# Performance work log

Hardware: AMD Instinct MI355X
Metric: run time of the kernel (lower is better)

The kernel has to match this reference:

```python
import jax, jax.numpy as jnp
import numpy as np

N = 50000      # num_nodes
R = 8          # num_relations
FIN = 128      # in_channels
H = 128        # hidden_channels
E = 800000     # num_edges (avg degree 16)


def _xavier(key, shape):
    fan_in, fan_out = shape[-2], shape[-1]
    lim = np.sqrt(6.0 / (fan_in + fan_out)).astype(np.float32)
    return jax.random.uniform(key, shape, jnp.float32, -lim, lim)


def setup_inputs() -> dict:
    key = jax.random.key(0)
    ks = jax.random.split(key, 10)
    return {
        "x": jax.random.normal(ks[0], (N, FIN), jnp.float32),
        "edge_index": jax.random.randint(ks[1], (2, E), 0, N, jnp.int32),
        "edge_type": jax.random.randint(ks[2], (E,), 0, R, jnp.int32),
        "rel_w0": _xavier(ks[3], (R, FIN, H)),
        "root_w0": _xavier(ks[4], (FIN, H)),
        "bias0": jnp.zeros((H,), jnp.float32),
        "rel_w1": _xavier(ks[5], (R, H, H)),
        "root_w1": _xavier(ks[6], (H, H)),
        "bias1": jnp.zeros((H,), jnp.float32),
        "rel_emb": _xavier(ks[7], (R, H)),
    }


def _rgcn_conv(x, src, dst, etype, rel_w, root_w, bias):
    # RGCNConv (PyG, aggr='mean'): out_i = root(x_i) + sum_r W_r * mean_{j in N_r(i)} x_j
    n = x.shape[0]
    seg = dst * R + etype                                   # fused (node, relation) segment id
    msgs = x[src]                                           # [E, F] gather
    sums = jax.ops.segment_sum(msgs, seg, num_segments=n * R)
    cnt = jax.ops.segment_sum(jnp.ones((src.shape[0], 1), x.dtype), seg, num_segments=n * R)
    mean = (sums / jnp.maximum(cnt, 1.0)).reshape(n, R, -1)  # [N, R, F]
    return jnp.einsum('nrf,rfh->nh', mean, rel_w) + x @ root_w + bias


def reference(x, edge_index, edge_type, rel_w0, root_w0, bias0,
              rel_w1, root_w1, bias1, rel_emb):
    src, dst = edge_index[0], edge_index[1]
    h = _rgcn_conv(x, src, dst, edge_type, rel_w0, root_w0, bias0)
    h = jax.nn.relu(h)  # dropout in eval mode (identity)
    h = _rgcn_conv(h, src, dst, edge_type, rel_w1, root_w1, bias1)
    return (h, rel_emb)
```

## Files before the change

kernel.cpp:

```cpp
#include <hip/hip_runtime.h>

typedef unsigned short ushort_t;
typedef __attribute__((ext_vector_type(8))) short short8;
typedef __attribute__((ext_vector_type(4))) float f32x4;
typedef __attribute__((ext_vector_type(4))) int int4v;

#define RNUM 8
#define FDIM 128
#define KDIM 1152

__device__ __forceinline__ float bf2f(ushort_t u) {
    union { unsigned int i; float f; } x;
    x.i = ((unsigned int)u) << 16;
    return x.f;
}
__device__ __forceinline__ ushort_t f2bf(float f) {
    union { float f; unsigned int i; } x;
    x.f = f;
    unsigned int u = x.i;
    u += 0x7fffu + ((u >> 16) & 1u);
    return (ushort_t)(u >> 16);
}

__device__ __forceinline__ void gl_lds16(const void* g, void* s) {
    __builtin_amdgcn_global_load_lds(
        (const __attribute__((address_space(1))) unsigned int*)g,
        (__attribute__((address_space(3))) unsigned int*)s, 16, 0, 0);
}


__global__ void init_head(int* __restrict__ head, int n) {
    int i = blockIdx.x * 256 + threadIdx.x;
    if (i < n) head[i] = -1;
}

__global__ void link_kernel(const int* __restrict__ src, const int* __restrict__ dst,
                            const int* __restrict__ et,
                            int* head, int2* __restrict__ meta, int E) {
    int i = blockIdx.x * 256 + threadIdx.x;
    if (i < E) {
        int seg = dst[i] * RNUM + et[i];
        int prev = atomicExch(&head[seg * 4 + (i & 3)], i);
        meta[i] = make_int2(src[i], prev);
    }
}


__global__ __launch_bounds__(256) void transpose_w(const float* __restrict__ rel_w,
                                                   const float* __restrict__ root_w,
                                                   ushort_t* __restrict__ Wt) {
    int r = blockIdx.x;
    const float* src = (r < 8) ? (rel_w + r * 16384) : root_w;
    __shared__ ushort_t t[128 * 130];
    for (int idx = threadIdx.x; idx < 16384; idx += 256)
        t[(idx >> 7) * 130 + (idx & 127)] = f2bf(src[idx]);
    __syncthreads();
    ushort_t* d = Wt + r * 16384;
    for (int idx = threadIdx.x; idx < 16384; idx += 256)
        d[idx] = t[(idx & 127) * 130 + (idx >> 7)];
}


__global__ void cast_x(const float* __restrict__ x, ushort_t* __restrict__ Mx, int total) {
    int i = (blockIdx.x * 256 + threadIdx.x) * 8;
    if (i >= total) return;
    float4 v0 = *(const float4*)(x + i);
    float4 v1 = *(const float4*)(x + i + 4);
    ushort_t o[8] = {f2bf(v0.x), f2bf(v0.y), f2bf(v0.z), f2bf(v0.w),
                     f2bf(v1.x), f2bf(v1.y), f2bf(v1.z), f2bf(v1.w)};
    int row = i >> 7, col = i & 127;
    *(int4v*)(Mx + (size_t)row * KDIM + 1024 + col) = *(int4v*)o;
}


__global__ __launch_bounds__(256) void seg_mean(const int4v* __restrict__ head4,
                                                const int2* __restrict__ meta,
                                                ushort_t* Mx, int NSEG) {
    int t = blockIdx.x * 256 + threadIdx.x;
    int seg = t >> 4;
    int l16 = t & 15;
    if (seg >= NSEG) return;
    const ushort_t* gbase = Mx + 1024 + (size_t)l16 * 8;

    float acc[8];
#pragma unroll
    for (int k = 0; k < 8; ++k) acc[k] = 0.f;

    int4v h4 = head4[seg];
    int j[4], s[4], n[4];
#pragma unroll
    for (int c = 0; c < 4; ++c) j[c] = h4[c];
#pragma unroll
    for (int c = 0; c < 4; ++c)
        if (j[c] >= 0) { int2 m = meta[j[c]]; s[c] = m.x; n[c] = m.y; }

    int cnt = 0;
    while ((j[0] & j[1] & j[2] & j[3]) >= 0) {
        int4v v[4];
#pragma unroll
        for (int c = 0; c < 4; ++c)
            if (j[c] >= 0) v[c] = *(const int4v*)(gbase + (size_t)s[c] * KDIM);
        int2 m2[4];
#pragma unroll
        for (int c = 0; c < 4; ++c)
            if (j[c] >= 0 && n[c] >= 0) m2[c] = meta[n[c]];
#pragma unroll
        for (int c = 0; c < 4; ++c) {
            if (j[c] >= 0) {
                const ushort_t* p = (const ushort_t*)&v[c];
#pragma unroll
                for (int k = 0; k < 8; ++k) acc[k] += bf2f(p[k]);
                ++cnt;
                j[c] = n[c];
                s[c] = m2[c].x;
                n[c] = m2[c].y;
            }
        }
    }

    float sc = (cnt > 0) ? 1.0f / (float)cnt : 0.f;
    ushort_t ov[8];
#pragma unroll
    for (int k = 0; k < 8; ++k) ov[k] = f2bf(acc[k] * sc);
    *(int4v*)(Mx + (size_t)(seg >> 3) * KDIM + (seg & 7) * 128 + l16 * 8) = *(int4v*)ov;
}


template <bool FINAL>
__global__ __launch_bounds__(256) void rgcn_gemm(
    const ushort_t* Mx, const ushort_t* __restrict__ Wt,
    const float* __restrict__ bias, float* __restrict__ outF,
    ushort_t* MxOut, int N) {
    __shared__ ushort_t As[128 * 128];
    __shared__ ushort_t Bs[128 * 128];
    int tid = threadIdx.x;
    int wid = tid >> 6, lane = tid & 63;
    int l16 = lane & 15, q = lane >> 4;
    int nodeBase = blockIdx.x * 128;

    f32x4 acc[2][8];
#pragma unroll
    for (int rt = 0; rt < 2; ++rt)
#pragma unroll
        for (int ct = 0; ct < 8; ++ct) acc[rt][ct] = (f32x4){0.f, 0.f, 0.f, 0.f};

    for (int r = 0; r < 9; ++r) {
        __syncthreads();
#pragma unroll
        for (int i = 0; i < 8; ++i) {
            int L = i * 256 + tid;
            int row = L >> 4;
            int c = (L & 15) ^ (row & 15);
            gl_lds16(Mx + (size_t)(nodeBase + row) * KDIM + r * 128 + c * 8,
                     (char*)As + (size_t)L * 16);
            gl_lds16(Wt + r * 16384 + row * 128 + c * 8,
                     (char*)Bs + (size_t)L * 16);
        }
        __syncthreads();
#pragma unroll
        for (int s = 0; s < 4; ++s) {
            int pos = ((s * 4 + q) ^ l16) * 16;
            short8 a0 = *(const short8*)((const char*)As + ((2 * wid + 0) * 16 + l16) * 256 + pos);
            short8 a1 = *(const short8*)((const char*)As + ((2 * wid + 1) * 16 + l16) * 256 + pos);
#pragma unroll
            for (int ct = 0; ct < 8; ++ct) {
                short8 b = *(const short8*)((const char*)Bs + (ct * 16 + l16) * 256 + pos);
                acc[0][ct] = __builtin_amdgcn_mfma_f32_16x16x32_bf16(a0, b, acc[0][ct], 0, 0, 0);
                acc[1][ct] = __builtin_amdgcn_mfma_f32_16x16x32_bf16(a1, b, acc[1][ct], 0, 0, 0);
            }
        }
    }
#pragma unroll
    for (int rt = 0; rt < 2; ++rt) {
#pragma unroll
        for (int ct = 0; ct < 8; ++ct) {
            int h = ct * 16 + l16;
            float bv = bias[h];
#pragma unroll
            for (int reg = 0; reg < 4; ++reg) {
                int node = nodeBase + (2 * wid + rt) * 16 + q * 4 + reg;
                if (node < N) {
                    float v = acc[rt][ct][reg] + bv;
                    if (FINAL) {
                        outF[(size_t)node * FDIM + h] = v;
                    } else {
                        v = fmaxf(v, 0.f);
                        MxOut[(size_t)node * KDIM + 1024 + h] = f2bf(v);
                    }
                }
            }
        }
    }
}

__global__ void copy_emb(const float* __restrict__ e, float* __restrict__ out, int n) {
    int i = blockIdx.x * 256 + threadIdx.x;
    if (i < n) out[i] = e[i];
}


extern "C" void kernel_launch(void* const* d_in, const int* in_sizes, int n_in,
                              void* d_out, int out_size, void* d_ws, size_t ws_size,
                              hipStream_t stream) {
    const float* x        = (const float*)d_in[0];
    const int* edge_index = (const int*)d_in[1];
    const int* edge_type  = (const int*)d_in[2];
    const float* rel_w0   = (const float*)d_in[3];
    const float* root_w0  = (const float*)d_in[4];
    const float* bias0    = (const float*)d_in[5];
    const float* rel_w1   = (const float*)d_in[6];
    const float* root_w1  = (const float*)d_in[7];
    const float* bias1    = (const float*)d_in[8];
    const float* rel_emb  = (const float*)d_in[9];

    int N = in_sizes[0] / FDIM;
    int E = in_sizes[1] / 2;
    int NSEG = N * RNUM;
    const int* src = edge_index;
    const int* dst = edge_index + E;

    int nb_gemm = (N + 127) / 128;
    int NPAD = nb_gemm * 128;

    char* w = (char*)d_ws;
    auto alloc = [&](size_t bytes) -> char* {
        char* p = w;
        w += (bytes + 255) & ~(size_t)255;
        return p;
    };
    int* head    = (int*)alloc((size_t)NSEG * 4 * 4);
    int2* meta   = (int2*)alloc((size_t)E * 8);
    ushort_t* Wt = (ushort_t*)alloc((size_t)2 * 9 * 16384 * 2);
    ushort_t* Mx = (ushort_t*)alloc((size_t)NPAD * KDIM * 2);
    (void)ws_size; (void)n_in; (void)out_size;

    int nb_head = (NSEG * 4 + 255) / 256;
    int nb_E    = (E + 255) / 256;
    int nb_mean = (NSEG * 16) / 256;
    int nb_cast = (N * FDIM) / (256 * 8);

    init_head<<<nb_head, 256, 0, stream>>>(head, NSEG * 4);
    link_kernel<<<nb_E, 256, 0, stream>>>(src, dst, edge_type, head, meta, E);
    transpose_w<<<9, 256, 0, stream>>>(rel_w0, root_w0, Wt);
    transpose_w<<<9, 256, 0, stream>>>(rel_w1, root_w1, Wt + 9 * 16384);
    cast_x<<<nb_cast, 256, 0, stream>>>(x, Mx, N * FDIM);

    seg_mean<<<nb_mean, 256, 0, stream>>>((const int4v*)head, meta, Mx, NSEG);
    rgcn_gemm<false><<<nb_gemm, 256, 0, stream>>>(Mx, Wt, bias0, nullptr, Mx, N);
    seg_mean<<<nb_mean, 256, 0, stream>>>((const int4v*)head, meta, Mx, NSEG);
    rgcn_gemm<true><<<nb_gemm, 256, 0, stream>>>(Mx, Wt + 9 * 16384, bias1,
                                                 (float*)d_out, nullptr, N);
    copy_emb<<<4, 256, 0, stream>>>(rel_emb, (float*)d_out + (size_t)N * FDIM,
                                    in_sizes[9]);
}
```

Baseline: 323.9 us.

## Split node features from mean buffer, prefetch GEMM tiles via registers, branchless gather

Node features now sit in their own compact 128-wide bf16 array instead of inside a 1152-wide combined row, so seg_mean gathers from a denser buffer. The segment means go to a separate buffer. seg_mean's linked-list walk becomes branchless: finished lanes read a sentinel meta entry and an all-zero row instead of branching. The GEMM swaps its direct global-to-LDS loads for register-staged double buffering, so the next relation's tile is fetched during the MFMAs, with launch bounds set for two blocks per CU. This adds register pressure and extra wasted loads for lanes whose lists have already ended.

```diff
diff --git a/kernel.cpp b/kernel.cpp
--- a/kernel.cpp
+++ b/kernel.cpp
@@ -7,7 +7,6 @@
 
 #define RNUM 8
 #define FDIM 128
-#define KDIM 1152
 
 __device__ __forceinline__ float bf2f(ushort_t u) {
     union { unsigned int i; float f; } x;
@@ -22,26 +21,23 @@
     return (ushort_t)(u >> 16);
 }
 
-__device__ __forceinline__ void gl_lds16(const void* g, void* s) {
-    __builtin_amdgcn_global_load_lds(
-        (const __attribute__((address_space(1))) unsigned int*)g,
-        (__attribute__((address_space(3))) unsigned int*)s, 16, 0, 0);
-}
-
-
-__global__ void init_head(int* __restrict__ head, int n) {
+
+__global__ void init_head(int* __restrict__ head, int n, ushort_t* __restrict__ sent) {
     int i = blockIdx.x * 256 + threadIdx.x;
     if (i < n) head[i] = -1;
+    if (blockIdx.x == 0 && threadIdx.x < FDIM) sent[threadIdx.x] = 0;
 }
 
 __global__ void link_kernel(const int* __restrict__ src, const int* __restrict__ dst,
                             const int* __restrict__ et,
-                            int* head, int2* __restrict__ meta, int E) {
+                            int* head, int2* __restrict__ meta, int E, int zrow) {
     int i = blockIdx.x * 256 + threadIdx.x;
     if (i < E) {
         int seg = dst[i] * RNUM + et[i];
         int prev = atomicExch(&head[seg * 4 + (i & 3)], i);
         meta[i] = make_int2(src[i], prev);
+    } else if (i == E) {
+        meta[E] = make_int2(zrow, -1);
     }
 }
 
@@ -61,26 +57,34 @@
 }
 
 
-__global__ void cast_x(const float* __restrict__ x, ushort_t* __restrict__ Mx, int total) {
+__global__ void cast_x(const float* __restrict__ x, ushort_t* __restrict__ xc,
+                       int total, int totalPad) {
     int i = (blockIdx.x * 256 + threadIdx.x) * 8;
-    if (i >= total) return;
-    float4 v0 = *(const float4*)(x + i);
-    float4 v1 = *(const float4*)(x + i + 4);
-    ushort_t o[8] = {f2bf(v0.x), f2bf(v0.y), f2bf(v0.z), f2bf(v0.w),
-                     f2bf(v1.x), f2bf(v1.y), f2bf(v1.z), f2bf(v1.w)};
-    int row = i >> 7, col = i & 127;
-    *(int4v*)(Mx + (size_t)row * KDIM + 1024 + col) = *(int4v*)o;
+    if (i >= totalPad) return;
+    ushort_t o[8];
+    if (i < total) {
+        float4 v0 = *(const float4*)(x + i);
+        float4 v1 = *(const float4*)(x + i + 4);
+        o[0] = f2bf(v0.x); o[1] = f2bf(v0.y); o[2] = f2bf(v0.z); o[3] = f2bf(v0.w);
+        o[4] = f2bf(v1.x); o[5] = f2bf(v1.y); o[6] = f2bf(v1.z); o[7] = f2bf(v1.w);
+    } else {
+#pragma unroll
+        for (int k = 0; k < 8; ++k) o[k] = 0;
+    }
+    *(int4v*)(xc + i) = *(int4v*)o;
 }
 
 
 __global__ __launch_bounds__(256) void seg_mean(const int4v* __restrict__ head4,
                                                 const int2* __restrict__ meta,
-                                                ushort_t* Mx, int NSEG) {
+                                                const ushort_t* __restrict__ X,
+                                                ushort_t* __restrict__ Mm,
+                                                int NSEG, int E, int zrow) {
     int t = blockIdx.x * 256 + threadIdx.x;
     int seg = t >> 4;
     int l16 = t & 15;
     if (seg >= NSEG) return;
-    const ushort_t* gbase = Mx + 1024 + (size_t)l16 * 8;
+    const ushort_t* gbase = X + l16 * 8;
 
     float acc[8];
 #pragma unroll
@@ -91,30 +95,31 @@
 #pragma unroll
     for (int c = 0; c < 4; ++c) j[c] = h4[c];
 #pragma unroll
-    for (int c = 0; c < 4; ++c)
-        if (j[c] >= 0) { int2 m = meta[j[c]]; s[c] = m.x; n[c] = m.y; }
-
+    for (int c = 0; c < 4; ++c) {
+        int2 m = meta[(j[c] >= 0) ? j[c] : E];
+        s[c] = m.x; n[c] = m.y;
+    }
     int cnt = 0;
     while ((j[0] & j[1] & j[2] & j[3]) >= 0) {
         int4v v[4];
 #pragma unroll
+        for (int c = 0; c < 4; ++c) {
+            int row = (j[c] >= 0) ? s[c] : zrow;
+            v[c] = *(const int4v*)(gbase + ((size_t)row << 7));
+        }
+        int2 m2[4];
+#pragma unroll
         for (int c = 0; c < 4; ++c)
-            if (j[c] >= 0) v[c] = *(const int4v*)(gbase + (size_t)s[c] * KDIM);
-        int2 m2[4];
-#pragma unroll
-        for (int c = 0; c < 4; ++c)
-            if (j[c] >= 0 && n[c] >= 0) m2[c] = meta[n[c]];
+            m2[c] = meta[(n[c] >= 0) ? n[c] : E];
 #pragma unroll
         for (int c = 0; c < 4; ++c) {
-            if (j[c] >= 0) {
-                const ushort_t* p = (const ushort_t*)&v[c];
-#pragma unroll
-                for (int k = 0; k < 8; ++k) acc[k] += bf2f(p[k]);
-                ++cnt;
-                j[c] = n[c];
-                s[c] = m2[c].x;
-                n[c] = m2[c].y;
-            }
+            const ushort_t* p = (const ushort_t*)&v[c];
+#pragma unroll
+            for (int k = 0; k < 8; ++k) acc[k] += bf2f(p[k]);
+            cnt += (j[c] >= 0) ? 1 : 0;
+            j[c] = (j[c] >= 0) ? n[c] : -1;
+            s[c] = m2[c].x;
+            n[c] = m2[c].y;
         }
     }
 
@@ -122,15 +127,17 @@
     ushort_t ov[8];
 #pragma unroll
     for (int k = 0; k < 8; ++k) ov[k] = f2bf(acc[k] * sc);
-    *(int4v*)(Mx + (size_t)(seg >> 3) * KDIM + (seg & 7) * 128 + l16 * 8) = *(int4v*)ov;
+    *(int4v*)(Mm + ((size_t)seg << 7) + l16 * 8) = *(int4v*)ov;
 }
 
 
 template <bool FINAL>
-__global__ __launch_bounds__(256) void rgcn_gemm(
-    const ushort_t* Mx, const ushort_t* __restrict__ Wt,
+__global__ __launch_bounds__(256, 2) void rgcn_gemm(
+    const ushort_t* __restrict__ Mm,
+    const ushort_t* __restrict__ Xc,
+    const ushort_t* __restrict__ Wt,
     const float* __restrict__ bias, float* __restrict__ outF,
-    ushort_t* MxOut, int N) {
+    ushort_t* __restrict__ Xout, int N) {
     __shared__ ushort_t As[128 * 128];
     __shared__ ushort_t Bs[128 * 128];
     int tid = threadIdx.x;
@@ -144,19 +151,36 @@
 #pragma unroll
         for (int ct = 0; ct < 8; ++ct) acc[rt][ct] = (f32x4){0.f, 0.f, 0.f, 0.f};
 
-    for (int r = 0; r < 9; ++r) {
-        __syncthreads();
+    int4v aReg[8], bReg[8];
+
+    auto issueLoads = [&](int r) {
 #pragma unroll
         for (int i = 0; i < 8; ++i) {
             int L = i * 256 + tid;
             int row = L >> 4;
             int c = (L & 15) ^ (row & 15);
-            gl_lds16(Mx + (size_t)(nodeBase + row) * KDIM + r * 128 + c * 8,
-                     (char*)As + (size_t)L * 16);
-            gl_lds16(Wt + r * 16384 + row * 128 + c * 8,
-                     (char*)Bs + (size_t)L * 16);
-        }
-        __syncthreads();
+            const ushort_t* ga = (r < 8)
+                ? Mm + ((size_t)(nodeBase + row) << 10) + r * 128 + c * 8
+                : Xc + ((size_t)(nodeBase + row) << 7) + c * 8;
+            aReg[i] = *(const int4v*)ga;
+            bReg[i] = *(const int4v*)(Wt + r * 16384 + row * 128 + c * 8);
+        }
+    };
+    auto writeLds = [&]() {
+#pragma unroll
+        for (int i = 0; i < 8; ++i) {
+            int L = i * 256 + tid;
+            *(int4v*)((char*)As + (size_t)L * 16) = aReg[i];
+            *(int4v*)((char*)Bs + (size_t)L * 16) = bReg[i];
+        }
+    };
+
+    issueLoads(0);
+    writeLds();
+    __syncthreads();
+
+    for (int r = 0; r < 9; ++r) {
+        if (r < 8) issueLoads(r + 1);
 #pragma unroll
         for (int s = 0; s < 4; ++s) {
             int pos = ((s * 4 + q) ^ l16) * 16;
@@ -169,7 +193,13 @@
                 acc[1][ct] = __builtin_amdgcn_mfma_f32_16x16x32_bf16(a1, b, acc[1][ct], 0, 0, 0);
             }
         }
-    }
+        __syncthreads();
+        if (r < 8) {
+            writeLds();
+            __syncthreads();
+        }
+    }
+
 #pragma unroll
     for (int rt = 0; rt < 2; ++rt) {
 #pragma unroll
@@ -179,14 +209,12 @@
 #pragma unroll
             for (int reg = 0; reg < 4; ++reg) {
                 int node = nodeBase + (2 * wid + rt) * 16 + q * 4 + reg;
-                if (node < N) {
-                    float v = acc[rt][ct][reg] + bv;
-                    if (FINAL) {
-                        outF[(size_t)node * FDIM + h] = v;
-                    } else {
-                        v = fmaxf(v, 0.f);
-                        MxOut[(size_t)node * KDIM + 1024 + h] = f2bf(v);
-                    }
+                float v = acc[rt][ct][reg] + bv;
+                if (FINAL) {
+                    if (node < N) outF[(size_t)node * FDIM + h] = v;
+                } else {
+                    Xout[(size_t)node * FDIM + h] =
+                        (node < N) ? f2bf(fmaxf(v, 0.f)) : (ushort_t)0;
                 }
             }
         }
@@ -228,27 +256,31 @@
         w += (bytes + 255) & ~(size_t)255;
         return p;
     };
-    int* head    = (int*)alloc((size_t)NSEG * 4 * 4);
-    int2* meta   = (int2*)alloc((size_t)E * 8);
-    ushort_t* Wt = (ushort_t*)alloc((size_t)2 * 9 * 16384 * 2);
-    ushort_t* Mx = (ushort_t*)alloc((size_t)NPAD * KDIM * 2);
+    int* head     = (int*)alloc((size_t)NSEG * 4 * 4);
+    int2* meta    = (int2*)alloc((size_t)(E + 1) * 8);
+    ushort_t* Wt  = (ushort_t*)alloc((size_t)2 * 9 * 16384 * 2);
+    ushort_t* xc  = (ushort_t*)alloc((size_t)(NPAD + 1) * FDIM * 2);
+    ushort_t* h1c = (ushort_t*)alloc((size_t)(NPAD + 1) * FDIM * 2);
+    ushort_t* Mm  = (ushort_t*)alloc((size_t)NPAD * RNUM * FDIM * 2);
     (void)ws_size; (void)n_in; (void)out_size;
 
+    int ZROW = NPAD;
+
     int nb_head = (NSEG * 4 + 255) / 256;
-    int nb_E    = (E + 255) / 256;
+    int nb_E    = (E + 1 + 255) / 256;
     int nb_mean = (NSEG * 16) / 256;
-    int nb_cast = (N * FDIM) / (256 * 8);
-
-    init_head<<<nb_head, 256, 0, stream>>>(head, NSEG * 4);
-    link_kernel<<<nb_E, 256, 0, stream>>>(src, dst, edge_type, head, meta, E);
+    int nb_cast = ((NPAD + 1) * FDIM + 2047) / 2048;
+
+    init_head<<<nb_head, 256, 0, stream>>>(head, NSEG * 4, h1c + (size_t)NPAD * FDIM);
+    link_kernel<<<nb_E, 256, 0, stream>>>(src, dst, edge_type, head, meta, E, ZROW);
     transpose_w<<<9, 256, 0, stream>>>(rel_w0, root_w0, Wt);
     transpose_w<<<9, 256, 0, stream>>>(rel_w1, root_w1, Wt + 9 * 16384);
-    cast_x<<<nb_cast, 256, 0, stream>>>(x, Mx, N * FDIM);
-
-    seg_mean<<<nb_mean, 256, 0, stream>>>((const int4v*)head, meta, Mx, NSEG);
-    rgcn_gemm<false><<<nb_gemm, 256, 0, stream>>>(Mx, Wt, bias0, nullptr, Mx, N);
-    seg_mean<<<nb_mean, 256, 0, stream>>>((const int4v*)head, meta, Mx, NSEG);
-    rgcn_gemm<true><<<nb_gemm, 256, 0, stream>>>(Mx, Wt + 9 * 16384, bias1,
+    cast_x<<<nb_cast, 256, 0, stream>>>(x, xc, N * FDIM, (NPAD + 1) * FDIM);
+
+    seg_mean<<<nb_mean, 256, 0, stream>>>((const int4v*)head, meta, xc, Mm, NSEG, E, ZROW);
+    rgcn_gemm<false><<<nb_gemm, 256, 0, stream>>>(Mm, xc, Wt, bias0, nullptr, h1c, N);
+    seg_mean<<<nb_mean, 256, 0, stream>>>((const int4v*)head, meta, h1c, Mm, NSEG, E, ZROW);
+    rgcn_gemm<true><<<nb_gemm, 256, 0, stream>>>(Mm, h1c, Wt + 9 * 16384, bias1,
                                                  (float*)d_out, nullptr, N);
     copy_emb<<<4, 256, 0, stream>>>(rel_emb, (float*)d_out + (size_t)N * FDIM,
                                     in_sizes[9]);
```

New measurement: 334.3 us. 1.03x slower.
